# Optimization experiments

Measured on AMD Instinct MI355X. Metric: run time of the kernel, lower is better.

Reference implementation:

```python
import jax, jax.numpy as jnp
import numpy as np

E, D, H = 8, 2048, 2048  # num_experts, features, expert_dim
B, L, K = 2, 2048, 2


def setup_inputs() -> dict:
    key = jax.random.key(0)
    k1, k2, k3, k4, k5, k6 = jax.random.split(key, 6)
    x = jax.random.normal(k1, (B, L, D), dtype=jnp.float32)
    w = jax.random.uniform(k2, (B, L, K), dtype=jnp.float32)
    weights = w / jnp.sum(w, axis=-1, keepdims=True)  # normalised routing weights
    expert_indices = jax.random.randint(k3, (B, L, K), 0, E, dtype=jnp.int64)
    gate_up = jax.random.normal(k4, (E, D, 2 * H), dtype=jnp.float32) * 0.02
    down = jax.random.normal(k5, (E, H, D), dtype=jnp.float32) * 0.02
    per_expert_scale = 1.0 + 0.01 * jax.random.normal(k6, (E,), dtype=jnp.float32)
    return {"x": x, "weights": weights, "expert_indices": expert_indices,
            "gate_up": gate_up, "down": down, "per_expert_scale": per_expert_scale}


def reference(x, weights, expert_indices, gate_up, down, per_expert_scale):
    Bb, Ll, Dd = x.shape
    Ee = gate_up.shape[0]
    N = Bb * Ll
    xf = x.reshape(N, Dd)                                   # [N, D]
    idx = expert_indices.reshape(N, -1)                     # [N, K]
    wts = weights.reshape(N, -1)                            # [N, K]
    # combine[n, e] = sum_k weights[n,k] * 1[idx[n,k]==e]; scale folded in.
    onehot = jax.nn.one_hot(idx, Ee, dtype=x.dtype)         # [N, K, E]
    combine = jnp.einsum('nk,nke->ne', wts, onehot) * per_expert_scale  # [N, E]
    # Dense per-expert GatedMLP (grouped GEMM across all experts).
    h = jnp.einsum('nd,edh->enh', xf, gate_up)              # [E, N, 2H]
    gate, up = jnp.split(h, 2, axis=-1)
    act = jax.nn.gelu(gate, approximate=False) * up         # exact gelu, as torch F.gelu
    y = jnp.einsum('enh,ehd->end', act, down)               # [E, N, D]
    out = jnp.einsum('end,ne->nd', y, combine)              # weighted combine over experts
    return out.reshape(Bb, Ll, Dd)
```

## Files before the change

### kernel.cpp

```cpp
#include <hip/hip_runtime.h>
#include <math.h>

#define EXPERTS 8
#define DDIM 2048
#define HDIM 2048
#define NTOK 4096
#define NPAIR 8192
#define MAXSLOT 9216
#define MAXTILE 72

typedef _Float16 f16;
typedef __attribute__((ext_vector_type(8))) _Float16 f16x8;
typedef __attribute__((ext_vector_type(4))) _Float16 f16x4;
typedef __attribute__((ext_vector_type(4))) float f32x4;

#define XF_OFF   0ull
#define ACT_OFF  16777216ull
#define Y_OFF    54525952ull
#define CTRL_OFF 92274688ull
#define CTRL_INTS 26792

#define BARRIER() asm volatile("s_barrier" ::: "memory")
#define VMCNT(n)  asm volatile("s_waitcnt vmcnt(" #n ")" ::: "memory")
#define LGKM0()   asm volatile("s_waitcnt lgkmcnt(0)" ::: "memory")

__device__ __forceinline__ void gload_lds16(const void* g, void* l) {
  __builtin_amdgcn_global_load_lds(
      (const __attribute__((address_space(1))) unsigned int*)g,
      (__attribute__((address_space(3))) unsigned int*)l,
      16, 0, 0);
}

__global__ void k_detect(const int* __restrict__ w, int* flag) {
  int i = blockIdx.x * blockDim.x + threadIdx.x;
  if (i < NPAIR / 2 && w[2 * i + 1] != 0) atomicOr(flag, 1);
}

__device__ __forceinline__ int expert_of(const int* idx, int is32, int p) {
  return is32 ? idx[p] : idx[2 * p];
}

__global__ void k_count(const int* __restrict__ idx, const int* __restrict__ flag,
                        int* cnt) {
  int p = blockIdx.x * blockDim.x + threadIdx.x;
  if (p < NPAIR) atomicAdd(&cnt[expert_of(idx, *flag, p)], 1);
}

__global__ void k_plan(const int* __restrict__ cnt, int* cursor,
                       int* tile_e, int* tile_r0, int* n_tiles) {
  if (blockIdx.x == 0 && threadIdx.x == 0) {
    int off = 0, nt = 0;
    for (int e = 0; e < EXPERTS; ++e) {
      cursor[e] = off;
      int t = (cnt[e] + 127) >> 7;
      for (int i = 0; i < t; ++i) { tile_e[nt] = e; tile_r0[nt] = off + i * 128; ++nt; }
      off += t * 128;
    }
    *n_tiles = nt;
  }
}

__global__ void k_assign(const int* __restrict__ idx, const int* __restrict__ flag,
                         const float* __restrict__ wts, const float* __restrict__ scale,
                         int* cursor, int* slot_tok, int* tok_slot, float* slot_w) {
  int p = blockIdx.x * blockDim.x + threadIdx.x;
  if (p < NPAIR) {
    int e = expert_of(idx, *flag, p);
    int pos = atomicAdd(&cursor[e], 1);
    slot_tok[pos] = p >> 1;
    tok_slot[p] = pos;
    slot_w[pos] = wts[p] * scale[e];
  }
}

__global__ void k_cvt_x(const float* __restrict__ in, f16* __restrict__ out) {
  int i = blockIdx.x * blockDim.x + threadIdx.x;
  float4 v = ((const float4*)in)[i];
  f16x4 o = {(f16)v.x, (f16)v.y, (f16)v.z, (f16)v.w};
  ((f16x4*)out)[i] = o;
}

template <int G1>
__global__ __launch_bounds__(512, 2) void k_gemm(
    const f16* __restrict__ Asrc, const float* __restrict__ W,
    const int* __restrict__ slot_tok,
    const int* __restrict__ tile_e, const int* __restrict__ tile_r0,
    const int* __restrict__ n_tiles, f16* __restrict__ dst) {
  __shared__ __align__(16) f16 smem[2][16384];

  const int bx = blockIdx.y;
  if (bx >= *n_tiles) return;
  const int nt = blockIdx.x;
  const int e = tile_e[bx];
  const int m0 = tile_r0[bx];
  const int LDB = G1 ? 4096 : 2048;

  const int tid = threadIdx.x;
  const int lane = tid & 63;
  const int wv = tid >> 6;
  const int wrM = wv >> 2;
  const int wcl = wv & 3;
  const int fr = lane & 15;
  const int fhi = lane >> 4;

  const f16* aS[2];
#pragma unroll
  for (int i = 0; i < 2; ++i) {
    const int r = i * 64 + (tid >> 3);
    size_t arow = G1 ? (size_t)slot_tok[m0 + r] : (size_t)(m0 + r);
    aS[i] = Asrc + arow * 2048 + ((tid & 7) ^ (r & 7)) * 8;
  }
  auto gloadA = [&](int s, int kt) {
#pragma unroll
    for (int i = 0; i < 2; ++i)
      gload_lds16(aS[i] + (size_t)kt * 64, &smem[s][i * 4096 + tid * 8]);
  };

  const int cp = tid & 63;
  const int kf = tid >> 6;
  int gcol;
  if (G1) gcol = (cp < 32) ? nt * 64 + 2 * cp : 2048 + nt * 64 + (2 * cp - 64);
  else    gcol = nt * 128 + 2 * cp;
  const float* bP = W + (size_t)e * 2048 * LDB + (size_t)(8 * kf) * LDB + gcol;
  const int bbase = 8192 + 2 * cp * 64 + ((kf ^ (cp & 7)) << 3);

  float2 q[8];
  auto loadB = [&](int kt) {
    const float* p = bP + (size_t)kt * 64 * LDB;
#pragma unroll
    for (int j = 0; j < 8; ++j) q[j] = *(const float2*)(p + j * LDB);
  };
  auto writeB = [&](int s) {
    f16x8 wa = {(f16)q[0].x, (f16)q[1].x, (f16)q[2].x, (f16)q[3].x,
                (f16)q[4].x, (f16)q[5].x, (f16)q[6].x, (f16)q[7].x};
    f16x8 wb = {(f16)q[0].y, (f16)q[1].y, (f16)q[2].y, (f16)q[3].y,
                (f16)q[4].y, (f16)q[5].y, (f16)q[6].y, (f16)q[7].y};
    *(f16x8*)&smem[s][bbase] = wa;
    *(f16x8*)&smem[s][bbase + 64] = wb;
  };

  int ctv[2];
#pragma unroll
  for (int ci = 0; ci < 2; ++ci)
    ctv[ci] = G1 ? (wcl + ci * 4) : (wcl * 2 + ci);

  f32x4 acc[4][2];
#pragma unroll
  for (int i = 0; i < 4; ++i)
#pragma unroll
    for (int j = 0; j < 2; ++j) acc[i][j] = (f32x4){0.f, 0.f, 0.f, 0.f};

  auto compute = [&](int s) {
    const f16* As = &smem[s][0];
    const f16* Bs = &smem[s][0];
    f16x8 af[4][2], bf[2][2];
#pragma unroll
    for (int mi = 0; mi < 4; ++mi)
#pragma unroll
      for (int k0 = 0; k0 < 2; ++k0) {
        const int r = wrM * 64 + mi * 16 + fr;
        af[mi][k0] = *(const f16x8*)&As[r * 64 + (((k0 * 4 + fhi) ^ (r & 7)) << 3)];
      }
#pragma unroll
    for (int ci = 0; ci < 2; ++ci)
#pragma unroll
      for (int k0 = 0; k0 < 2; ++k0) {
        const int c = ctv[ci] * 16 + fr;
        bf[ci][k0] = *(const f16x8*)&Bs[8192 + c * 64 +
                                        (((k0 * 4 + fhi) ^ ((c >> 1) & 7)) << 3)];
      }
    __builtin_amdgcn_s_setprio(1);
#pragma unroll
    for (int k0 = 0; k0 < 2; ++k0)
#pragma unroll
      for (int mi = 0; mi < 4; ++mi)
#pragma unroll
        for (int ci = 0; ci < 2; ++ci)
          acc[mi][ci] = __builtin_amdgcn_mfma_f32_16x16x32_f16(
              af[mi][k0], bf[ci][k0], acc[mi][ci], 0, 0, 0);
    __builtin_amdgcn_s_setprio(0);
  };

  const int NT = 32;

  loadB(0);
  gloadA(0, 0);
  VMCNT(2);
  writeB(0);
  __builtin_amdgcn_sched_barrier(0);
  loadB(1);
  VMCNT(8);
  LGKM0();
  BARRIER();

  for (int kt = 0; kt < NT; ++kt) {
    const int s = kt & 1;
    if (kt + 1 < NT) {
      gloadA(s ^ 1, kt + 1);
      VMCNT(2);
      writeB(s ^ 1);
      __builtin_amdgcn_sched_barrier(0);
      if (kt + 2 < NT) loadB(kt + 2);
    }
    compute(s);
    if (kt + 1 < NT) {
      if (kt + 2 < NT) { VMCNT(8); } else { VMCNT(0); }
      LGKM0();
      BARRIER();
    }
  }

  if (G1) {
#pragma unroll
    for (int mi = 0; mi < 4; ++mi)
#pragma unroll
      for (int rg = 0; rg < 4; ++rg) {
        const int row = m0 + wrM * 64 + mi * 16 + fhi * 4 + rg;
        const int col = nt * 64 + wcl * 16 + fr;
        const float g = acc[mi][0][rg];
        const float u = acc[mi][1][rg];
        const float a = 0.5f * g * (1.0f + erff(g * 0.70710678118654752f)) * u;
        dst[(size_t)row * 2048 + col] = (f16)a;
      }
  } else {
#pragma unroll
    for (int mi = 0; mi < 4; ++mi)
#pragma unroll
      for (int ci = 0; ci < 2; ++ci)
#pragma unroll
        for (int rg = 0; rg < 4; ++rg) {
          const int row = m0 + wrM * 64 + mi * 16 + fhi * 4 + rg;
          const int col = nt * 128 + (wcl * 2 + ci) * 16 + fr;
          dst[(size_t)row * 2048 + col] = (f16)acc[mi][ci][rg];
        }
  }
}

__global__ void k_combine(const f16* __restrict__ y, const float* __restrict__ slot_w,
                          const int* __restrict__ tok_slot, float* __restrict__ out) {
  const int gid = blockIdx.x * blockDim.x + threadIdx.x;
  const int tok = gid >> 8;
  const int c = (gid & 255) * 8;
  const int s0 = tok_slot[2 * tok], s1 = tok_slot[2 * tok + 1];
  const float w0 = slot_w[s0], w1 = slot_w[s1];
  const f16x8 v0 = *(const f16x8*)&y[(size_t)s0 * 2048 + c];
  const f16x8 v1 = *(const f16x8*)&y[(size_t)s1 * 2048 + c];
  float o[8];
#pragma unroll
  for (int j = 0; j < 8; ++j) o[j] = w0 * (float)v0[j] + w1 * (float)v1[j];
  float4* op = (float4*)&out[(size_t)tok * 2048 + c];
  op[0] = (float4){o[0], o[1], o[2], o[3]};
  op[1] = (float4){o[4], o[5], o[6], o[7]};
}

extern "C" void kernel_launch(void* const* d_in, const int* in_sizes, int n_in,
                              void* d_out, int out_size, void* d_ws, size_t ws_size,
                              hipStream_t stream) {
  const float* x = (const float*)d_in[0];
  const float* wts = (const float*)d_in[1];
  const int* idx = (const int*)d_in[2];
  const float* gup = (const float*)d_in[3];
  const float* dwn = (const float*)d_in[4];
  const float* scale = (const float*)d_in[5];
  float* out = (float*)d_out;

  char* ws = (char*)d_ws;
  f16* xf = (f16*)(ws + XF_OFF);
  f16* act = (f16*)(ws + ACT_OFF);
  f16* y = (f16*)(ws + Y_OFF);
  int* ctrl = (int*)(ws + CTRL_OFF);
  int* slot_tok = ctrl;
  int* tok_slot = ctrl + 9216;
  int* cnt = ctrl + 17408;
  int* cursor = ctrl + 17416;
  int* tile_e = ctrl + 17424;
  int* tile_r0 = ctrl + 17496;
  int* n_tiles = ctrl + 17568;
  int* is32 = ctrl + 17569;
  float* slot_w = (float*)(ctrl + 17576);

  hipMemsetAsync(ctrl, 0, (size_t)CTRL_INTS * sizeof(int), stream);

  k_detect<<<NPAIR / 2 / 256, 256, 0, stream>>>(idx, is32);
  k_count<<<NPAIR / 256, 256, 0, stream>>>(idx, is32, cnt);
  k_plan<<<1, 1, 0, stream>>>(cnt, cursor, tile_e, tile_r0, n_tiles);
  k_assign<<<NPAIR / 256, 256, 0, stream>>>(idx, is32, wts, scale, cursor,
                                            slot_tok, tok_slot, slot_w);
  k_cvt_x<<<NTOK * DDIM / 4 / 256, 256, 0, stream>>>(x, xf);
  k_gemm<1><<<dim3(32, MAXTILE), 512, 0, stream>>>(xf, gup, slot_tok, tile_e,
                                                   tile_r0, n_tiles, act);
  k_gemm<0><<<dim3(16, MAXTILE), 512, 0, stream>>>(act, dwn, slot_tok, tile_e,
                                                   tile_r0, n_tiles, y);
  k_combine<<<NTOK, 256, 0, stream>>>(y, slot_w, tok_slot, out);
}
```

Baseline: 487.5 us.

## Pre-transpose expert weights to f16 and stage B via direct LDS loads

Adds a transpose kernel that converts gate_up and down weights to fp16, K-contiguous layouts before each grouped GEMM. The GEMM then loads B tiles with global_load_lds instead of strided fp32 register loads plus in-register conversion and LDS writes, and restructures the k-loop so the next B stage is issued mid-compute. It also remaps block ids so neighbouring blocks share B column tiles for cache reuse. The cost is an extra full pass over the weights each call (read fp32, write fp16) and more workspace, with y aliasing the gate_up transposed buffer.

```diff
diff --git a/kernel.cpp b/kernel.cpp
--- a/kernel.cpp
+++ b/kernel.cpp
@@ -14,15 +14,16 @@
 typedef __attribute__((ext_vector_type(4))) _Float16 f16x4;
 typedef __attribute__((ext_vector_type(4))) float f32x4;
 
-#define XF_OFF   0ull
-#define ACT_OFF  16777216ull
-#define Y_OFF    54525952ull
-#define CTRL_OFF 92274688ull
+#define GUPT_OFF 0ull
+#define Y_OFF    0ull
+#define DWNT_OFF 41943040ull
+#define XF_OFF   134217728ull
+#define ACT_OFF  150994944ull
+#define CTRL_OFF 192937984ull
 #define CTRL_INTS 26792
 
 #define BARRIER() asm volatile("s_barrier" ::: "memory")
 #define VMCNT(n)  asm volatile("s_waitcnt vmcnt(" #n ")" ::: "memory")
-#define LGKM0()   asm volatile("s_waitcnt lgkmcnt(0)" ::: "memory")
 
 __device__ __forceinline__ void gload_lds16(const void* g, void* l) {
   __builtin_amdgcn_global_load_lds(
@@ -80,20 +81,49 @@
   ((f16x4*)out)[i] = o;
 }
 
+__global__ __launch_bounds__(256) void k_transpose(const float* __restrict__ in,
+                                                   f16* __restrict__ out,
+                                                   int R, int C) {
+  __shared__ float t[64][65];
+  const size_t base = (size_t)blockIdx.z * R * C;
+  const float* ip = in + base;
+  f16* op = out + base;
+  const int c0 = blockIdx.x * 64, r0 = blockIdx.y * 64;
+  const int tid = threadIdx.x;
+  const int rr = tid >> 4, cc = (tid & 15) * 4;
+#pragma unroll
+  for (int i = 0; i < 4; ++i) {
+    float4 v = *(const float4*)&ip[(size_t)(r0 + rr + i * 16) * C + c0 + cc];
+    *(float4*)&t[rr + i * 16][cc] = v;
+  }
+  __syncthreads();
+  const int k0 = (tid & 7) * 8;
+#pragma unroll
+  for (int p = 0; p < 2; ++p) {
+    const int j = (tid >> 3) + p * 32;
+    f16x8 w = {(f16)t[k0 + 0][j], (f16)t[k0 + 1][j], (f16)t[k0 + 2][j],
+               (f16)t[k0 + 3][j], (f16)t[k0 + 4][j], (f16)t[k0 + 5][j],
+               (f16)t[k0 + 6][j], (f16)t[k0 + 7][j]};
+    *(f16x8*)&op[(size_t)(c0 + j) * R + r0 + k0] = w;
+  }
+}
+
 template <int G1>
 __global__ __launch_bounds__(512, 2) void k_gemm(
-    const f16* __restrict__ Asrc, const float* __restrict__ W,
+    const f16* __restrict__ Asrc, const f16* __restrict__ Bsrc,
     const int* __restrict__ slot_tok,
     const int* __restrict__ tile_e, const int* __restrict__ tile_r0,
     const int* __restrict__ n_tiles, f16* __restrict__ dst) {
   __shared__ __align__(16) f16 smem[2][16384];
 
-  const int bx = blockIdx.y;
+  const int NTX = G1 ? 32 : 16;
+  const int GP = NTX / 8;
+  const int oid = (int)(blockIdx.y * NTX + blockIdx.x);
+  const int nt = (oid & 7) * GP + ((oid >> 3) & (GP - 1));
+  const int bx = oid >> (G1 ? 5 : 4);
   if (bx >= *n_tiles) return;
-  const int nt = blockIdx.x;
   const int e = tile_e[bx];
   const int m0 = tile_r0[bx];
-  const int LDB = G1 ? 4096 : 2048;
 
   const int tid = threadIdx.x;
   const int lane = tid & 63;
@@ -103,40 +133,30 @@
   const int fr = lane & 15;
   const int fhi = lane >> 4;
 
+  const int sr = tid >> 3;
+  const int sc = (tid & 7) ^ (sr & 7);
   const f16* aS[2];
+  const f16* bS[2];
 #pragma unroll
   for (int i = 0; i < 2; ++i) {
-    const int r = i * 64 + (tid >> 3);
+    const int r = i * 64 + sr;
     size_t arow = G1 ? (size_t)slot_tok[m0 + r] : (size_t)(m0 + r);
-    aS[i] = Asrc + arow * 2048 + ((tid & 7) ^ (r & 7)) * 8;
-  }
-  auto gloadA = [&](int s, int kt) {
+    aS[i] = Asrc + arow * 2048 + sc * 8;
+    size_t brow;
+    if (G1) brow = (size_t)e * 4096 + (i ? (size_t)(2048 + nt * 64 + sr)
+                                         : (size_t)(nt * 64 + sr));
+    else    brow = (size_t)e * 2048 + nt * 128 + r;
+    bS[i] = Bsrc + brow * 2048 + sc * 8;
+  }
+  auto stageA = [&](int s, int kt) {
 #pragma unroll
     for (int i = 0; i < 2; ++i)
       gload_lds16(aS[i] + (size_t)kt * 64, &smem[s][i * 4096 + tid * 8]);
   };
-
-  const int cp = tid & 63;
-  const int kf = tid >> 6;
-  int gcol;
-  if (G1) gcol = (cp < 32) ? nt * 64 + 2 * cp : 2048 + nt * 64 + (2 * cp - 64);
-  else    gcol = nt * 128 + 2 * cp;
-  const float* bP = W + (size_t)e * 2048 * LDB + (size_t)(8 * kf) * LDB + gcol;
-  const int bbase = 8192 + 2 * cp * 64 + ((kf ^ (cp & 7)) << 3);
-
-  float2 q[8];
-  auto loadB = [&](int kt) {
-    const float* p = bP + (size_t)kt * 64 * LDB;
-#pragma unroll
-    for (int j = 0; j < 8; ++j) q[j] = *(const float2*)(p + j * LDB);
-  };
-  auto writeB = [&](int s) {
-    f16x8 wa = {(f16)q[0].x, (f16)q[1].x, (f16)q[2].x, (f16)q[3].x,
-                (f16)q[4].x, (f16)q[5].x, (f16)q[6].x, (f16)q[7].x};
-    f16x8 wb = {(f16)q[0].y, (f16)q[1].y, (f16)q[2].y, (f16)q[3].y,
-                (f16)q[4].y, (f16)q[5].y, (f16)q[6].y, (f16)q[7].y};
-    *(f16x8*)&smem[s][bbase] = wa;
-    *(f16x8*)&smem[s][bbase + 64] = wb;
+  auto stageB = [&](int s, int kt) {
+#pragma unroll
+    for (int i = 0; i < 2; ++i)
+      gload_lds16(bS[i] + (size_t)kt * 64, &smem[s][8192 + i * 4096 + tid * 8]);
   };
 
   int ctv[2];
@@ -150,62 +170,66 @@
 #pragma unroll
     for (int j = 0; j < 2; ++j) acc[i][j] = (f32x4){0.f, 0.f, 0.f, 0.f};
 
-  auto compute = [&](int s) {
+  const int NT = 32;
+
+  stageB(0, 0);
+  stageA(0, 0);
+  stageB(1, 1);
+  VMCNT(2);
+  BARRIER();
+
+  for (int kt = 0; kt < NT; ++kt) {
+    const int s = kt & 1;
+    if (kt + 1 < NT) stageA(s ^ 1, kt + 1);
+
     const f16* As = &smem[s][0];
-    const f16* Bs = &smem[s][0];
-    f16x8 af[4][2], bf[2][2];
-#pragma unroll
-    for (int mi = 0; mi < 4; ++mi)
+    const f16* Bs = &smem[s][8192];
+    f16x8 bf[2][2];
+#pragma unroll
+    for (int ci = 0; ci < 2; ++ci)
+#pragma unroll
+      for (int k0 = 0; k0 < 2; ++k0) {
+        const int c = ctv[ci] * 16 + fr;
+        bf[ci][k0] = *(const f16x8*)&Bs[c * 64 + (((k0 * 4 + fhi) ^ (c & 7)) << 3)];
+      }
+#pragma unroll
+    for (int mi = 0; mi < 2; ++mi) {
+      f16x8 af[2];
 #pragma unroll
       for (int k0 = 0; k0 < 2; ++k0) {
         const int r = wrM * 64 + mi * 16 + fr;
-        af[mi][k0] = *(const f16x8*)&As[r * 64 + (((k0 * 4 + fhi) ^ (r & 7)) << 3)];
+        af[k0] = *(const f16x8*)&As[r * 64 + (((k0 * 4 + fhi) ^ (r & 7)) << 3)];
       }
-#pragma unroll
-    for (int ci = 0; ci < 2; ++ci)
+      __builtin_amdgcn_s_setprio(1);
+#pragma unroll
+      for (int ci = 0; ci < 2; ++ci)
+#pragma unroll
+        for (int k0 = 0; k0 < 2; ++k0)
+          acc[mi][ci] = __builtin_amdgcn_mfma_f32_16x16x32_f16(
+              af[k0], bf[ci][k0], acc[mi][ci], 0, 0, 0);
+      __builtin_amdgcn_s_setprio(0);
+    }
+    BARRIER();
+    if (kt + 2 < NT) stageB(s, kt + 2);
+#pragma unroll
+    for (int mi = 2; mi < 4; ++mi) {
+      f16x8 af[2];
 #pragma unroll
       for (int k0 = 0; k0 < 2; ++k0) {
-        const int c = ctv[ci] * 16 + fr;
-        bf[ci][k0] = *(const f16x8*)&Bs[8192 + c * 64 +
-                                        (((k0 * 4 + fhi) ^ ((c >> 1) & 7)) << 3)];
+        const int r = wrM * 64 + mi * 16 + fr;
+        af[k0] = *(const f16x8*)&As[r * 64 + (((k0 * 4 + fhi) ^ (r & 7)) << 3)];
       }
-    __builtin_amdgcn_s_setprio(1);
-#pragma unroll
-    for (int k0 = 0; k0 < 2; ++k0)
-#pragma unroll
-      for (int mi = 0; mi < 4; ++mi)
-#pragma unroll
-        for (int ci = 0; ci < 2; ++ci)
+      __builtin_amdgcn_s_setprio(1);
+#pragma unroll
+      for (int ci = 0; ci < 2; ++ci)
+#pragma unroll
+        for (int k0 = 0; k0 < 2; ++k0)
           acc[mi][ci] = __builtin_amdgcn_mfma_f32_16x16x32_f16(
-              af[mi][k0], bf[ci][k0], acc[mi][ci], 0, 0, 0);
-    __builtin_amdgcn_s_setprio(0);
-  };
-
-  const int NT = 32;
-
-  loadB(0);
-  gloadA(0, 0);
-  VMCNT(2);
-  writeB(0);
-  __builtin_amdgcn_sched_barrier(0);
-  loadB(1);
-  VMCNT(8);
-  LGKM0();
-  BARRIER();
-
-  for (int kt = 0; kt < NT; ++kt) {
-    const int s = kt & 1;
+              af[k0], bf[ci][k0], acc[mi][ci], 0, 0, 0);
+      __builtin_amdgcn_s_setprio(0);
+    }
     if (kt + 1 < NT) {
-      gloadA(s ^ 1, kt + 1);
-      VMCNT(2);
-      writeB(s ^ 1);
-      __builtin_amdgcn_sched_barrier(0);
-      if (kt + 2 < NT) loadB(kt + 2);
-    }
-    compute(s);
-    if (kt + 1 < NT) {
-      if (kt + 2 < NT) { VMCNT(8); } else { VMCNT(0); }
-      LGKM0();
+      if (kt + 2 < NT) { VMCNT(2); } else { VMCNT(0); }
       BARRIER();
     }
   }
@@ -265,9 +289,11 @@
   float* out = (float*)d_out;
 
   char* ws = (char*)d_ws;
+  f16* gup_t = (f16*)(ws + GUPT_OFF);
+  f16* y = (f16*)(ws + Y_OFF);
+  f16* down_t = (f16*)(ws + DWNT_OFF);
   f16* xf = (f16*)(ws + XF_OFF);
   f16* act = (f16*)(ws + ACT_OFF);
-  f16* y = (f16*)(ws + Y_OFF);
   int* ctrl = (int*)(ws + CTRL_OFF);
   int* slot_tok = ctrl;
   int* tok_slot = ctrl + 9216;
@@ -287,9 +313,13 @@
   k_assign<<<NPAIR / 256, 256, 0, stream>>>(idx, is32, wts, scale, cursor,
                                             slot_tok, tok_slot, slot_w);
   k_cvt_x<<<NTOK * DDIM / 4 / 256, 256, 0, stream>>>(x, xf);
-  k_gemm<1><<<dim3(32, MAXTILE), 512, 0, stream>>>(xf, gup, slot_tok, tile_e,
+  k_transpose<<<dim3(4096 / 64, 2048 / 64, EXPERTS), 256, 0, stream>>>(
+      gup, gup_t, 2048, 4096);
+  k_gemm<1><<<dim3(32, MAXTILE), 512, 0, stream>>>(xf, gup_t, slot_tok, tile_e,
                                                    tile_r0, n_tiles, act);
-  k_gemm<0><<<dim3(16, MAXTILE), 512, 0, stream>>>(act, dwn, slot_tok, tile_e,
+  k_transpose<<<dim3(2048 / 64, 2048 / 64, EXPERTS), 256, 0, stream>>>(
+      dwn, down_t, 2048, 2048);
+  k_gemm<0><<<dim3(16, MAXTILE), 512, 0, stream>>>(act, down_t, slot_tok, tile_e,
                                                    tile_r0, n_tiles, y);
   k_combine<<<NTOK, 256, 0, stream>>>(y, slot_w, tok_slot, out);
 }
```

Result: faster. 461.9 us (median of 2 runs) (-5.3%).

## Deepen B-prefetch to two stages and remap tile order for L2 reuse

Applied to the files above, without the earlier changes.

Uses two register buffers for the fp32 weight tiles so global loads run two k-steps ahead, and removes the wait between the A async load and the B store to LDS. Also remaps the block index so that consecutive blocks share the same weight columns across row tiles, which should improve L2 reuse of the expert weights. The cost is more registers per thread, which may hurt occupancy at launch bounds of 512 threads with 2 blocks per CU, and the vmcnt bookkeeping becomes more fragile.

```diff
diff --git a/kernel.cpp b/kernel.cpp
--- a/kernel.cpp
+++ b/kernel.cpp
@@ -88,9 +88,12 @@
     const int* __restrict__ n_tiles, f16* __restrict__ dst) {
   __shared__ __align__(16) f16 smem[2][16384];
 
-  const int bx = blockIdx.y;
+  const int NTX = G1 ? 32 : 16;
+  const int GP = NTX / 8;
+  const int oid = (int)(blockIdx.y * NTX + blockIdx.x);
+  const int nt = (oid & 7) * GP + ((oid >> 3) & (GP - 1));
+  const int bx = oid >> (G1 ? 5 : 4);
   if (bx >= *n_tiles) return;
-  const int nt = blockIdx.x;
   const int e = tile_e[bx];
   const int m0 = tile_r0[bx];
   const int LDB = G1 ? 4096 : 2048;
@@ -124,13 +127,13 @@
   const float* bP = W + (size_t)e * 2048 * LDB + (size_t)(8 * kf) * LDB + gcol;
   const int bbase = 8192 + 2 * cp * 64 + ((kf ^ (cp & 7)) << 3);
 
-  float2 q[8];
-  auto loadB = [&](int kt) {
+  float2 qe[8], qo[8];
+  auto loadB = [&](float2 (&q)[8], int kt) {
     const float* p = bP + (size_t)kt * 64 * LDB;
 #pragma unroll
     for (int j = 0; j < 8; ++j) q[j] = *(const float2*)(p + j * LDB);
   };
-  auto writeB = [&](int s) {
+  auto writeB = [&](float2 (&q)[8], int s) {
     f16x8 wa = {(f16)q[0].x, (f16)q[1].x, (f16)q[2].x, (f16)q[3].x,
                 (f16)q[4].x, (f16)q[5].x, (f16)q[6].x, (f16)q[7].x};
     f16x8 wb = {(f16)q[0].y, (f16)q[1].y, (f16)q[2].y, (f16)q[3].y,
@@ -152,7 +155,7 @@
 
   auto compute = [&](int s) {
     const f16* As = &smem[s][0];
-    const f16* Bs = &smem[s][0];
+    const f16* Bs = &smem[s][8192];
     f16x8 af[4][2], bf[2][2];
 #pragma unroll
     for (int mi = 0; mi < 4; ++mi)
@@ -166,8 +169,7 @@
 #pragma unroll
       for (int k0 = 0; k0 < 2; ++k0) {
         const int c = ctv[ci] * 16 + fr;
-        bf[ci][k0] = *(const f16x8*)&Bs[8192 + c * 64 +
-                                        (((k0 * 4 + fhi) ^ ((c >> 1) & 7)) << 3)];
+        bf[ci][k0] = *(const f16x8*)&Bs[c * 64 + (((k0 * 4 + fhi) ^ ((c >> 1) & 7)) << 3)];
       }
     __builtin_amdgcn_s_setprio(1);
 #pragma unroll
@@ -183,31 +185,35 @@
 
   const int NT = 32;
 
-  loadB(0);
+  loadB(qe, 0);
+  loadB(qo, 1);
   gloadA(0, 0);
-  VMCNT(2);
-  writeB(0);
+  VMCNT(10);
+  writeB(qe, 0);
   __builtin_amdgcn_sched_barrier(0);
-  loadB(1);
+  loadB(qe, 2);
   VMCNT(8);
   LGKM0();
   BARRIER();
 
-  for (int kt = 0; kt < NT; ++kt) {
+  auto giter = [&](int kt, float2 (&Q)[8]) {
     const int s = kt & 1;
     if (kt + 1 < NT) {
+      writeB(Q, s ^ 1);
       gloadA(s ^ 1, kt + 1);
-      VMCNT(2);
-      writeB(s ^ 1);
       __builtin_amdgcn_sched_barrier(0);
-      if (kt + 2 < NT) loadB(kt + 2);
+      if (kt + 3 < NT) loadB(Q, kt + 3);
     }
     compute(s);
     if (kt + 1 < NT) {
-      if (kt + 2 < NT) { VMCNT(8); } else { VMCNT(0); }
+      if (kt + 3 < NT) { VMCNT(8); } else { VMCNT(0); }
       LGKM0();
       BARRIER();
     }
+  };
+  for (int kt = 0; kt < NT; kt += 2) {
+    giter(kt, qo);
+    giter(kt + 1, qe);
   }
 
   if (G1) {
```

New measurement: 611.9 us. 1.26x slower.
